# Performance work log

Hardware: AMD Instinct MI355X
Metric: run time of the kernel (lower is better)

## Reference

```python
import jax, jax.numpy as jnp
import numpy as np

B, T, IMG, PS, D, DEPTH, NH = 1, 8, 224, 16, 768, 12, 12
HP = IMG // PS
NP = HP * HP          # 196 patches per frame
N = NP + 1            # +1 cls token per frame
DH = D // NH
MLP = 4 * D
SCALE = DH ** -0.5


def _ln(x, g, b):
    mu = x.mean(-1, keepdims=True)
    var = ((x - mu) ** 2).mean(-1, keepdims=True)
    return (x - mu) / jnp.sqrt(var + 1e-5) * g + b


def _forward(x, W_patch, b_patch, cls_token, pos_embed,
             ln1_g, ln1_b, qkv_w, qkv_b, proj_w, proj_b,
             ln2_g, ln2_b, fc1_w, fc1_b, fc2_w, fc2_b, lnf_g, lnf_b):
    Bc = x.shape[0]
    # --- patch embed (Conv3d k=(1,ps,ps), stride=(1,ps,ps) == per-frame patch matmul) ---
    p = x.reshape(Bc, T, 3, HP, PS, HP, PS).transpose(0, 1, 3, 5, 2, 4, 6)
    p = p.reshape(Bc, T, NP, 3 * PS * PS)
    emb = p @ W_patch.T + b_patch                     # [B,T,NP,D] (correct layout)
    # replicate torch flatten(3)/transpose(1,2)/reshape axis scramble:
    emb = jnp.swapaxes(emb, 2, 3).reshape(Bc, T, NP, D)
    cls = jnp.broadcast_to(cls_token.reshape(1, 1, 1, D), (Bc, T, 1, D))
    h = jnp.concatenate([cls, emb], axis=2) + pos_embed.reshape(1, 1, N, D)
    h = h.reshape(Bc, T * N, D)

    for i in range(DEPTH):
        # --- attention ---
        a = _ln(h, ln1_g[i], ln1_b[i])
        qkv = (a @ qkv_w[i] + qkv_b[i]).reshape(Bc, T * N, 3, NH, DH)
        q, k, v = (jnp.transpose(qkv[:, :, j], (0, 2, 1, 3)) for j in range(3))  # [B,H,S,dh]
        if i % 2 == 0:  # divided space-time
            qf = q.reshape(Bc, NH, T, N, DH)
            kf = k.reshape(Bc, NH, T, N, DH)
            vf = v.reshape(Bc, NH, T, N, DH)
            q_t = qf.mean(3, keepdims=True)           # [B,H,T,1,dh]
            k_t = kf.mean(3, keepdims=True)
            v_t = vf.mean(3, keepdims=True)
            attn_t = jax.nn.softmax(jnp.einsum('bhtqd,bhtkd->bhtqk', q_t, k_t) * SCALE, -1)
            x_t = jnp.einsum('bhtqk,bhtkd->bhtqd', attn_t, v_t)[:, :, :, 0]  # [B,H,T,dh]
            attn_s = jax.nn.softmax(jnp.einsum('bhtqd,bhtkd->bhtqk', qf, kf) * SCALE, -1)
            x_s = jnp.einsum('bhtqk,bhtkd->bhtqd', attn_s, vf)               # [B,H,T,N,dh]
            o = (x_s + x_t[:, :, :, None, :]).reshape(Bc, NH, T * N, DH)
        else:  # joint space-time
            attn = jax.nn.softmax(jnp.einsum('bhqd,bhkd->bhqk', q, k) * SCALE, -1)
            o = jnp.einsum('bhqk,bhkd->bhqd', attn, v)
        o = jnp.transpose(o, (0, 2, 1, 3)).reshape(Bc, T * N, D)
        h = h + (o @ proj_w[i] + proj_b[i])
        # --- mlp ---
        m = _ln(h, ln2_g[i], ln2_b[i])
        m = jax.nn.gelu(m @ fc1_w[i] + fc1_b[i], approximate=False)
        h = h + (m @ fc2_w[i] + fc2_b[i])

    return _ln(h, lnf_g, lnf_b).reshape(Bc, T, N, D)


def setup_inputs() -> dict:
    key = jax.random.key(0)
    ks = jax.random.split(key, 12)
    s = 0.02
    return {
        'x': jax.random.normal(ks[0], (B, T, 3, IMG, IMG), jnp.float32),
        'W_patch': jax.random.normal(ks[1], (D, 3 * PS * PS), jnp.float32) * s,
        'b_patch': jnp.zeros((D,), jnp.float32),
        'cls_token': jax.random.normal(ks[2], (1, 1, D), jnp.float32) * s,
        'pos_embed': jax.random.normal(ks[3], (1, N, D), jnp.float32) * s,
        'ln1_g': jnp.ones((DEPTH, D), jnp.float32),
        'ln1_b': jnp.zeros((DEPTH, D), jnp.float32),
        'qkv_w': jax.random.normal(ks[4], (DEPTH, D, 3 * D), jnp.float32) * s,
        'qkv_b': jnp.zeros((DEPTH, 3 * D), jnp.float32),
        'proj_w': jax.random.normal(ks[5], (DEPTH, D, D), jnp.float32) * s,
        'proj_b': jnp.zeros((DEPTH, D), jnp.float32),
        'ln2_g': jnp.ones((DEPTH, D), jnp.float32),
        'ln2_b': jnp.zeros((DEPTH, D), jnp.float32),
        'fc1_w': jax.random.normal(ks[6], (DEPTH, D, MLP), jnp.float32) * s,
        'fc1_b': jnp.zeros((DEPTH, MLP), jnp.float32),
        'fc2_w': jax.random.normal(ks[7], (DEPTH, MLP, D), jnp.float32) * s,
        'fc2_b': jnp.zeros((DEPTH, D), jnp.float32),
        'lnf_g': jnp.ones((D,), jnp.float32),
        'lnf_b': jnp.zeros((D,), jnp.float32),
    }


def reference(x, W_patch, b_patch, cls_token, pos_embed,
              ln1_g, ln1_b, qkv_w, qkv_b, proj_w, proj_b,
              ln2_g, ln2_b, fc1_w, fc1_b, fc2_w, fc2_b, lnf_g, lnf_b):
    return _forward(x, W_patch, b_patch, cls_token, pos_embed,
                    ln1_g, ln1_b, qkv_w, qkv_b, proj_w, proj_b,
                    ln2_g, ln2_b, fc1_w, fc1_b, fc2_w, fc2_b, lnf_g, lnf_b)
```

## Files before the change

kernel.cpp:

```cpp
#include <hip/hip_runtime.h>
#include <math.h>

#define Dm 768
#define Tn 8
#define Nn 197
#define Sn 1576
#define MLPn 3072
#define NPn 196
#define MPAD 1664

typedef unsigned short u16;
typedef __bf16 bf16x8 __attribute__((ext_vector_type(8)));
typedef float f32x4 __attribute__((ext_vector_type(4)));
typedef unsigned int u32x4 __attribute__((ext_vector_type(4)));
typedef u16 u16x8 __attribute__((ext_vector_type(8)));
typedef u16 u16x4 __attribute__((ext_vector_type(4)));

__device__ inline u16 f2bf(float f) {
    union { float f; unsigned u; } v; v.f = f;
    unsigned r = v.u + 0x7fffu + ((v.u >> 16) & 1u);
    return (u16)(r >> 16);
}
__device__ inline float bf2f(u16 v) {
    union { unsigned u; float f; } x; x.u = ((unsigned)v) << 16; return x.f;
}

__device__ __forceinline__ void gl_lds16(const u16* __restrict__ g, u16* l) {
    __builtin_amdgcn_global_load_lds((const __attribute__((address_space(1))) void*)g,
                                     (__attribute__((address_space(3))) void*)l,
                                     16, 0, 0);
}

__global__ __launch_bounds__(256) void im2col_k(const float* __restrict__ x, u16* __restrict__ P) {
    int idx = blockIdx.x * 256 + threadIdx.x;
    if (idx >= 1568 * 768) return;
    int c = idx % 768, r = idx / 768;
    int p = r % 196, t = r / 196;
    int hp = p / 14, wp = p % 14;
    int ch = c / 256, rem = c % 256, py = rem / 16, px = rem % 16;
    P[idx] = f2bf(x[((t * 3 + ch) * 224 + hp * 16 + py) * 224 + wp * 16 + px]);
}

__global__ __launch_bounds__(256) void cvt_k(const float* __restrict__ s, u16* __restrict__ d, int n) {
    int i = blockIdx.x * 256 + threadIdx.x;
    if (i < n) d[i] = f2bf(s[i]);
}

__global__ __launch_bounds__(256) void cvtT_all_k(const float* __restrict__ qw_, const float* __restrict__ pw_,
                                                  const float* __restrict__ f1w_, const float* __restrict__ f2w_,
                                                  u16* __restrict__ Wq_, u16* __restrict__ Wp_,
                                                  u16* __restrict__ W1_, u16* __restrict__ W2_) {
    __shared__ float tile[32][33];
    int layer = blockIdx.y;
    const float* qw  = qw_  + (size_t)layer * 768 * 2304;
    const float* pw  = pw_  + (size_t)layer * 768 * 768;
    const float* f1w = f1w_ + (size_t)layer * 768 * 3072;
    const float* f2w = f2w_ + (size_t)layer * 3072 * 768;
    u16* Wq = Wq_ + (size_t)layer * 2304 * 768;
    u16* Wp = Wp_ + (size_t)layer * 768 * 768;
    u16* W1 = W1_ + (size_t)layer * 3072 * 768;
    u16* W2 = W2_ + (size_t)layer * 768 * 3072;
    int bid = blockIdx.x;
    const float* src; u16* dst; int K, N, k0, n0;
    if (bid < 1728)      { src = qw;  dst = Wq; K = 768;  N = 2304; int r = bid;        k0 = (r / 72) * 32; n0 = (r % 72) * 32; }
    else if (bid < 2304) { src = pw;  dst = Wp; K = 768;  N = 768;  int r = bid - 1728; k0 = (r / 24) * 32; n0 = (r % 24) * 32; }
    else if (bid < 4608) { src = f1w; dst = W1; K = 768;  N = 3072; int r = bid - 2304; k0 = (r / 96) * 32; n0 = (r % 96) * 32; }
    else                 { src = f2w; dst = W2; K = 3072; N = 768;  int r = bid - 4608; k0 = (r / 24) * 32; n0 = (r % 24) * 32; }
    int tx = threadIdx.x & 31, ty = threadIdx.x >> 5;
#pragma unroll
    for (int i = 0; i < 4; ++i) tile[ty + 8 * i][tx] = src[(size_t)(k0 + ty + 8 * i) * N + n0 + tx];
    __syncthreads();
#pragma unroll
    for (int i = 0; i < 4; ++i) dst[(size_t)(n0 + ty + 8 * i) * K + k0 + tx] = f2bf(tile[tx][ty + 8 * i]);
}

__global__ __launch_bounds__(256) void build_h_k(const float* __restrict__ emb, const float* __restrict__ cls,
                                                 const float* __restrict__ pos, float* __restrict__ h) {
    int idx = blockIdx.x * 256 + threadIdx.x;
    if (idx >= Sn * Dm) return;
    int d = idx % Dm, s = idx / Dm;
    int t = s / Nn, r = s % Nn;
    float v;
    if (r == 0) v = cls[d];
    else {
        int f = (r - 1) * Dm + d;
        int p = f % NPn, dd = f / NPn;
        v = emb[(size_t)(t * NPn + p) * Dm + dd];
    }
    h[idx] = v + pos[r * Dm + d];
}

template <typename OutT>
__global__ __launch_bounds__(256) void ln_k(const float* __restrict__ X, const float* __restrict__ g,
                                            const float* __restrict__ bta, OutT* __restrict__ Y) {
    int row = blockIdx.x;
    const float* x = X + (size_t)row * Dm;
    float s = 0.f, s2 = 0.f;
#pragma unroll
    for (int q = 0; q < 3; ++q) {
        float v = x[threadIdx.x + q * 256];
        s += v; s2 += v * v;
    }
#pragma unroll
    for (int off = 1; off < 64; off <<= 1) {
        s  += __shfl_xor(s,  off);
        s2 += __shfl_xor(s2, off);
    }
    __shared__ float red[8];
    int wv = threadIdx.x >> 6;
    if ((threadIdx.x & 63) == 0) { red[wv * 2] = s; red[wv * 2 + 1] = s2; }
    __syncthreads();
    s  = red[0] + red[2] + red[4] + red[6];
    s2 = red[1] + red[3] + red[5] + red[7];
    float mu  = s * (1.f / 768.f);
    float var = s2 * (1.f / 768.f) - mu * mu;
    float rstd = rsqrtf(var + 1e-5f);
#pragma unroll
    for (int q = 0; q < 3; ++q) {
        int i = threadIdx.x + q * 256;
        float v = (x[i] - mu) * rstd * g[i] + bta[i];
        if constexpr (sizeof(OutT) == 2) Y[(size_t)row * Dm + i] = f2bf(v);
        else                             Y[(size_t)row * Dm + i] = v;
    }
}

__global__ __launch_bounds__(256) void mgemm_k(const u16* __restrict__ A, const u16* __restrict__ Bt,
                                               float* __restrict__ Cp, int N, int Kfull, int Kc) {
    __shared__ __align__(16) u16 As[3 * 4096];
    __shared__ __align__(16) u16 Bs[3 * 4096];
    int split = blockIdx.z;
    A  += split * Kc;
    Bt += split * Kc;
    Cp += (size_t)split * MPAD * N;
    int tid = threadIdx.x;
    int lane = tid & 63, w = tid >> 6;
    int wm = w & 1, wn = w >> 1;
    int m0 = blockIdx.y * 128, n0 = blockIdx.x * 128;
    f32x4 acc[4][4] = {};
    int c0 = tid, c1 = tid + 256;
    int ar0 = ((c0 >> 6) << 4) + (c0 & 15), ac0 = ((c0 >> 4) & 3) << 3;
    int ar1 = ((c1 >> 6) << 4) + (c1 & 15), ac1 = ((c1 >> 4) & 3) << 3;
    const u16* Arow0 = A  + (size_t)(m0 + ar0) * Kfull + ac0;
    const u16* Arow1 = A  + (size_t)(m0 + ar1) * Kfull + ac1;
    const u16* Brow0 = Bt + (size_t)(n0 + ar0) * Kfull + ac0;
    const u16* Brow1 = Bt + (size_t)(n0 + ar1) * Kfull + ac1;
    auto STAGE = [&](int buf, int k0) {
        int bo = buf * 4096;
        gl_lds16(Arow0 + k0, As + bo + (w * 64) * 8);
        gl_lds16(Arow1 + k0, As + bo + (256 + w * 64) * 8);
        gl_lds16(Brow0 + k0, Bs + bo + (w * 64) * 8);
        gl_lds16(Brow1 + k0, Bs + bo + (256 + w * 64) * 8);
    };
    int nt = Kc >> 5;
    STAGE(0, 0);
    STAGE(1, 32);
    int buf = 0;
    for (int t = 0; t < nt; ++t) {
        if (t + 2 < nt) { int sb = buf + 2; if (sb >= 3) sb -= 3; STAGE(sb, (t + 2) * 32); }
        int ahead = nt - 1 - t;
        if (ahead >= 2)      asm volatile("s_waitcnt vmcnt(8)" ::: "memory");
        else if (ahead == 1) asm volatile("s_waitcnt vmcnt(4)" ::: "memory");
        else                 asm volatile("s_waitcnt vmcnt(0)" ::: "memory");
        __builtin_amdgcn_s_barrier();
        const u16* Ab = As + buf * 4096;
        const u16* Bb = Bs + buf * 4096;
        bf16x8 af[4], bfr[4];
#pragma unroll
        for (int i = 0; i < 4; ++i) {
            af[i]  = *(const bf16x8*)(Ab + (((wm * 4 + i) * 64 + lane) << 3));
            bfr[i] = *(const bf16x8*)(Bb + (((wn * 4 + i) * 64 + lane) << 3));
        }
#pragma unroll
        for (int mi = 0; mi < 4; ++mi)
#pragma unroll
            for (int ni = 0; ni < 4; ++ni)
                acc[mi][ni] = __builtin_amdgcn_mfma_f32_16x16x32_bf16(af[mi], bfr[ni], acc[mi][ni], 0, 0, 0);
        asm volatile("" ::: "memory");
        __builtin_amdgcn_s_barrier();
        buf = (buf == 2) ? 0 : buf + 1;
    }
    int rbase = (lane >> 4) << 2, cl = lane & 15;
#pragma unroll
    for (int mi = 0; mi < 4; ++mi)
#pragma unroll
        for (int r = 0; r < 4; ++r) {
            int gm = m0 + wm * 64 + mi * 16 + rbase + r;
#pragma unroll
            for (int ni = 0; ni < 4; ++ni) {
                int gn = n0 + wn * 64 + ni * 16 + cl;
                Cp[(size_t)gm * N + gn] = acc[mi][ni][r];
            }
        }
}

template <bool GELU_ACT>
__global__ __launch_bounds__(256) void mgemm_fused_k(const u16* __restrict__ A, const u16* __restrict__ Bt,
                                                     const float* __restrict__ bias, u16* __restrict__ out,
                                                     int N, int Kfull, int Mout) {
    __shared__ __align__(16) u16 As[3 * 64 * 32];
    __shared__ __align__(16) u16 Bs[3 * 128 * 32];
    int tid = threadIdx.x;
    int lane = tid & 63, w = tid >> 6;
    int wm = w & 1, wn = w >> 1;
    int m0 = blockIdx.y * 64, n0 = blockIdx.x * 128;
    f32x4 acc[2][4] = {};
    int ca = tid;
    int ar = ((ca >> 6) << 4) + (ca & 15), ac = ((ca >> 4) & 3) << 3;
    const u16* Arow = A + (size_t)(m0 + ar) * Kfull + ac;
    int cb1 = tid + 256;
    int br1 = ((cb1 >> 6) << 4) + (cb1 & 15), bc1 = ((cb1 >> 4) & 3) << 3;
    const u16* Brow0 = Bt + (size_t)(n0 + ar) * Kfull + ac;
    const u16* Brow1 = Bt + (size_t)(n0 + br1) * Kfull + bc1;
    auto STAGE = [&](int buf, int k0) {
        gl_lds16(Arow + k0, As + buf * 2048 + (w * 64) * 8);
        gl_lds16(Brow0 + k0, Bs + buf * 4096 + (w * 64) * 8);
        gl_lds16(Brow1 + k0, Bs + buf * 4096 + (256 + w * 64) * 8);
    };
    int nt = Kfull >> 5;
    STAGE(0, 0);
    STAGE(1, 32);
    int buf = 0;
    for (int t = 0; t < nt; ++t) {
        if (t + 2 < nt) { int sb = buf + 2; if (sb >= 3) sb -= 3; STAGE(sb, (t + 2) * 32); }
        int ahead = nt - 1 - t;
        if (ahead >= 2)      asm volatile("s_waitcnt vmcnt(6)" ::: "memory");
        else if (ahead == 1) asm volatile("s_waitcnt vmcnt(3)" ::: "memory");
        else                 asm volatile("s_waitcnt vmcnt(0)" ::: "memory");
        __builtin_amdgcn_s_barrier();
        const u16* Ab = As + buf * 2048;
        const u16* Bb = Bs + buf * 4096;
        bf16x8 af[2], bfr[4];
#pragma unroll
        for (int i = 0; i < 2; ++i) af[i]  = *(const bf16x8*)(Ab + (((wm * 2 + i) * 64 + lane) << 3));
#pragma unroll
        for (int j = 0; j < 4; ++j) bfr[j] = *(const bf16x8*)(Bb + (((wn * 4 + j) * 64 + lane) << 3));
#pragma unroll
        for (int mi = 0; mi < 2; ++mi)
#pragma unroll
            for (int ni = 0; ni < 4; ++ni)
                acc[mi][ni] = __builtin_amdgcn_mfma_f32_16x16x32_bf16(af[mi], bfr[ni], acc[mi][ni], 0, 0, 0);
        asm volatile("" ::: "memory");
        __builtin_amdgcn_s_barrier();
        buf = (buf == 2) ? 0 : buf + 1;
    }
    int rbase = (lane >> 4) << 2, cl = lane & 15;
#pragma unroll
    for (int mi = 0; mi < 2; ++mi)
#pragma unroll
        for (int r = 0; r < 4; ++r) {
            int gm = m0 + wm * 32 + mi * 16 + rbase + r;
            if (gm < Mout) {
#pragma unroll
                for (int ni = 0; ni < 4; ++ni) {
                    int gn = n0 + wn * 64 + ni * 16 + cl;
                    float v = acc[mi][ni][r] + bias[gn];
                    if (GELU_ACT) v = 0.5f * v * (1.f + erff(v * 0.7071067811865476f));
                    out[(size_t)gm * N + gn] = f2bf(v);
                }
            }
        }
}

__global__ __launch_bounds__(256) void ep_k(const float* __restrict__ Cp, const float* __restrict__ bias,
                                            float* __restrict__ out, int N, int S) {
    int row = blockIdx.y;
    int n = blockIdx.x * 1024 + threadIdx.x * 4;
    if (n >= N) return;
    size_t off = (size_t)row * N + n;
    f32x4 acc = *(const f32x4*)(Cp + off);
    for (int s = 1; s < S; ++s)
        acc += *(const f32x4*)(Cp + (size_t)s * MPAD * N + off);
    acc += *(const f32x4*)(bias + n);
    *(f32x4*)(out + off) = acc;
}

template <bool FINALOUT>
__global__ __launch_bounds__(256) void ep_ln_k(const float* __restrict__ Cp, const float* __restrict__ bias,
                                               float* __restrict__ h, const float* __restrict__ g,
                                               const float* __restrict__ bta, void* __restrict__ lnout, int S) {
    int row = blockIdx.x;
    int t = threadIdx.x;
    float v[3];
    float s = 0.f, s2 = 0.f;
#pragma unroll
    for (int q = 0; q < 3; ++q) {
        int i = t + q * 256;
        size_t off = (size_t)row * Dm + i;
        float a = Cp[off];
        for (int sp = 1; sp < S; ++sp) a += Cp[(size_t)sp * MPAD * Dm + off];
        a += bias[i] + h[off];
        h[off] = a;
        v[q] = a; s += a; s2 += a * a;
    }
#pragma unroll
    for (int off = 1; off < 64; off <<= 1) {
        s  += __shfl_xor(s,  off);
        s2 += __shfl_xor(s2, off);
    }
    __shared__ float red[8];
    int wv = t >> 6;
    if ((t & 63) == 0) { red[wv * 2] = s; red[wv * 2 + 1] = s2; }
    __syncthreads();
    s  = red[0] + red[2] + red[4] + red[6];
    s2 = red[1] + red[3] + red[5] + red[7];
    float mu  = s * (1.f / 768.f);
    float var = s2 * (1.f / 768.f) - mu * mu;
    float rstd = rsqrtf(var + 1e-5f);
#pragma unroll
    for (int q = 0; q < 3; ++q) {
        int i = t + q * 256;
        float y = (v[q] - mu) * rstd * g[i] + bta[i];
        if constexpr (FINALOUT) ((float*)lnout)[(size_t)row * Dm + i] = y;
        else                    ((u16*)lnout)[(size_t)row * Dm + i] = f2bf(y);
    }
}

__global__ __launch_bounds__(256) void vmean_k(const u16* __restrict__ qkv, float* __restrict__ vm) {
    int g = blockIdx.x;
    int h = g >> 3, t = g & 7;
    int d = threadIdx.x & 63, part = threadIdx.x >> 6;
    float s = 0.f;
    for (int n = part; n < Nn; n += 4)
        s += bf2f(qkv[(size_t)(t * Nn + n) * 2304 + 1536 + h * 64 + d]);
    __shared__ float red[256];
    red[threadIdx.x] = s;
    __syncthreads();
    if (part == 0) vm[g * 64 + d] = (red[d] + red[64 + d] + red[128 + d] + red[192 + d]) * (1.f / 197.f);
}

__global__ __launch_bounds__(256) void attn_mfma_k(const u16* __restrict__ qkv, float* __restrict__ Ou,
                                                   float* __restrict__ ml, const float* __restrict__ vm,
                                                   u16* __restrict__ ob, int even, int nsplit,
                                                   int NG, int Sq, int fuse) {
    __shared__ __align__(16) u16 Ks[64 * 64];
    __shared__ __align__(16) u16 Vt[64 * 64];
    __shared__ __align__(16) u16 Ps[4 * 32 * 64];
    int g = blockIdx.y;
    int h, sbase;
    if (even) { h = g >> 3; sbase = (g & 7) * Nn; } else { h = g; sbase = 0; }
    int split = blockIdx.z;
    int chunk = (Sq + nsplit - 1) / nsplit;
    int kbeg = split * chunk, kend = min(Sq, kbeg + chunk);
    int tid = threadIdx.x, lane = tid & 63, w = tid >> 6;
    int quad = lane >> 4, l15 = lane & 15;
    int q0w = blockIdx.x * 128 + w * 32;
    u16* Pw = Ps + w * 2048;

    bf16x8 aq[2][2];
#pragma unroll
    for (int mb = 0; mb < 2; ++mb) {
        int qidx = q0w + mb * 16 + l15; if (qidx >= Sq) qidx = Sq - 1;
        const u16* qp = qkv + (size_t)(sbase + qidx) * 2304 + h * 64;
#pragma unroll
        for (int ks = 0; ks < 2; ++ks)
            aq[mb][ks] = *(const bf16x8*)(qp + ks * 32 + quad * 8);
    }
    f32x4 acc_o[2][4] = {};
    float m_run[2][4], l_run[2][4];
#pragma unroll
    for (int mb = 0; mb < 2; ++mb)
#pragma unroll
        for (int r = 0; r < 4; ++r) { m_run[mb][r] = -INFINITY; l_run[mb][r] = 0.f; }

    for (int kt = kbeg; kt < kend; kt += 64) {
        int cnt = kend - kt; if (cnt > 64) cnt = 64;
        {
            int dc = tid & 7;
#pragma unroll
            for (int p = 0; p < 2; ++p) {
                int row = (tid >> 3) + 32 * p;
                u32x4 kd = {};
                if (row < cnt) kd = *(const u32x4*)(qkv + (size_t)(sbase + kt + row) * 2304 + 768 + h * 64 + dc * 8);
                *(u32x4*)(Ks + row * 64 + ((dc ^ (row & 7)) << 3)) = kd;
            }
        }
        {
            int d = (tid & 31) * 2, kc = tid >> 5;
            u16x8 lo, hi;
#pragma unroll
            for (int i = 0; i < 8; ++i) {
                int key = kc * 8 + i;
                unsigned t = 0;
                if (key < cnt) t = *(const unsigned*)(qkv + (size_t)(sbase + kt + key) * 2304 + 1536 + h * 64 + d);
                lo[i] = (u16)(t & 0xffffu); hi[i] = (u16)(t >> 16);
            }
            *(u16x8*)(Vt + d * 64 + ((kc ^ (d & 7)) << 3)) = lo;
            *(u16x8*)(Vt + (d + 1) * 64 + ((kc ^ ((d + 1) & 7)) << 3)) = hi;
        }
        __syncthreads();
        f32x4 acc_s[2][4] = {};
#pragma unroll
        for (int ni = 0; ni < 4; ++ni) {
            int key = l15 + ni * 16;
#pragma unroll
            for (int ks = 0; ks < 2; ++ks) {
                bf16x8 bk = *(const bf16x8*)(Ks + key * 64 + ((((ks << 2) + quad) ^ (key & 7)) << 3));
                acc_s[0][ni] = __builtin_amdgcn_mfma_f32_16x16x32_bf16(aq[0][ks], bk, acc_s[0][ni], 0, 0, 0);
                acc_s[1][ni] = __builtin_amdgcn_mfma_f32_16x16x32_bf16(aq[1][ks], bk, acc_s[1][ni], 0, 0, 0);
            }
        }
#pragma unroll
        for (int mb = 0; mb < 2; ++mb) {
#pragma unroll
            for (int ni = 0; ni < 4; ++ni) {
                int keyabs = kt + l15 + ni * 16;
#pragma unroll
                for (int r = 0; r < 4; ++r) {
                    float sv = acc_s[mb][ni][r] * 0.125f;
                    if (keyabs >= kend) sv = -1e30f;
                    acc_s[mb][ni][r] = sv;
                }
            }
#pragma unroll
            for (int r = 0; r < 4; ++r) {
                float mx = fmaxf(fmaxf(acc_s[mb][0][r], acc_s[mb][1][r]), fmaxf(acc_s[mb][2][r], acc_s[mb][3][r]));
                mx = fmaxf(mx, __shfl_xor(mx, 1));
                mx = fmaxf(mx, __shfl_xor(mx, 2));
                mx = fmaxf(mx, __shfl_xor(mx, 4));
                mx = fmaxf(mx, __shfl_xor(mx, 8));
                float mnew = fmaxf(m_run[mb][r], mx);
                float pv[4], ps = 0.f;
#pragma unroll
                for (int ni = 0; ni < 4; ++ni) { pv[ni] = __expf(acc_s[mb][ni][r] - mnew); ps += pv[ni]; }
                ps += __shfl_xor(ps, 1);
                ps += __shfl_xor(ps, 2);
                ps += __shfl_xor(ps, 4);
                ps += __shfl_xor(ps, 8);
                float alpha = __expf(m_run[mb][r] - mnew);
                l_run[mb][r] = l_run[mb][r] * alpha + ps;
                m_run[mb][r] = mnew;
#pragma unroll
                for (int ni = 0; ni < 4; ++ni) acc_o[mb][ni][r] *= alpha;
                int prow = mb * 16 + quad * 4 + r;
#pragma unroll
                for (int ni = 0; ni < 4; ++ni) {
                    int key = l15 + ni * 16;
                    Pw[prow * 64 + (((key >> 3) ^ (prow & 7)) << 3) + (key & 7)] = f2bf(pv[ni]);
                }
            }
        }
        bf16x8 ap[2][2];
#pragma unroll
        for (int mb = 0; mb < 2; ++mb)
#pragma unroll
            for (int ks = 0; ks < 2; ++ks)
                ap[mb][ks] = *(const bf16x8*)(Pw + (mb * 16 + l15) * 64 + ((((ks << 2) + quad) ^ (l15 & 7)) << 3));
#pragma unroll
        for (int ni = 0; ni < 4; ++ni) {
            int d = l15 + ni * 16;
#pragma unroll
            for (int ks = 0; ks < 2; ++ks) {
                bf16x8 bv = *(const bf16x8*)(Vt + d * 64 + ((((ks << 2) + quad) ^ (d & 7)) << 3));
                acc_o[0][ni] = __builtin_amdgcn_mfma_f32_16x16x32_bf16(ap[0][ks], bv, acc_o[0][ni], 0, 0, 0);
                acc_o[1][ni] = __builtin_amdgcn_mfma_f32_16x16x32_bf16(ap[1][ks], bv, acc_o[1][ni], 0, 0, 0);
            }
        }
        __syncthreads();
    }
    if (fuse) {
#pragma unroll
        for (int mb = 0; mb < 2; ++mb)
#pragma unroll
            for (int r = 0; r < 4; ++r) {
                int q = q0w + mb * 16 + quad * 4 + r;
                if (q < Sq) {
                    float inv = 1.f / l_run[mb][r];
                    u16* op = ob + (size_t)(sbase + q) * Dm + h * 64;
#pragma unroll
                    for (int ni = 0; ni < 4; ++ni) {
                        int d = l15 + ni * 16;
                        op[d] = f2bf(acc_o[mb][ni][r] * inv + vm[g * 64 + d]);
                    }
                }
            }
    } else {
        size_t gb = ((size_t)split * NG + g) * Sq;
#pragma unroll
        for (int mb = 0; mb < 2; ++mb)
#pragma unroll
            for (int r = 0; r < 4; ++r) {
                int q = q0w + mb * 16 + quad * 4 + r;
                if (q < Sq) {
                    float* op = Ou + (gb + q) * 64;
#pragma unroll
                    for (int ni = 0; ni < 4; ++ni) op[l15 + ni * 16] = acc_o[mb][ni][r];
                    if (l15 == 0) {
                        ml[(gb + q) * 2]     = m_run[mb][r];
                        ml[(gb + q) * 2 + 1] = l_run[mb][r];
                    }
                }
            }
    }
}

__global__ __launch_bounds__(256) void comb_k(const float* __restrict__ Ou, const float* __restrict__ ml,
                                              u16* __restrict__ ob, int nsplit, int NG, int Sq) {
    int g = blockIdx.y;
    int q = blockIdx.x * 4 + (threadIdx.x >> 6);
    int d = threadIdx.x & 63;
    if (q >= Sq) return;
    int h = g, sbase = 0;
    float M = -INFINITY;
    for (int s = 0; s < nsplit; ++s) M = fmaxf(M, ml[(((size_t)s * NG + g) * Sq + q) * 2]);
    float num = 0.f, den = 0.f;
    for (int s = 0; s < nsplit; ++s) {
        size_t base = ((size_t)s * NG + g) * Sq + q;
        float wgt = __expf(ml[base * 2] - M);
        den += wgt * ml[base * 2 + 1];
        num += wgt * Ou[base * 64 + d];
    }
    float o = num / den;
    ob[(size_t)(sbase + q) * Dm + h * 64 + d] = f2bf(o);
}

extern "C" void kernel_launch(void* const* d_in, const int* in_sizes, int n_in,
                              void* d_out, int out_size, void* d_ws, size_t ws_size,
                              hipStream_t stream) {
    (void)in_sizes; (void)n_in; (void)out_size; (void)ws_size;
    const float* x       = (const float*)d_in[0];
    const float* W_patch = (const float*)d_in[1];
    const float* b_patch = (const float*)d_in[2];
    const float* cls     = (const float*)d_in[3];
    const float* pos     = (const float*)d_in[4];
    const float* ln1_g   = (const float*)d_in[5];
    const float* ln1_b   = (const float*)d_in[6];
    const float* qkv_w   = (const float*)d_in[7];
    const float* qkv_b   = (const float*)d_in[8];
    const float* proj_w  = (const float*)d_in[9];
    const float* proj_b  = (const float*)d_in[10];
    const float* ln2_g   = (const float*)d_in[11];
    const float* ln2_b   = (const float*)d_in[12];
    const float* fc1_w   = (const float*)d_in[13];
    const float* fc1_b   = (const float*)d_in[14];
    const float* fc2_w   = (const float*)d_in[15];
    const float* fc2_b   = (const float*)d_in[16];
    const float* lnf_g   = (const float*)d_in[17];
    const float* lnf_b   = (const float*)d_in[18];

    char* base = (char*)d_ws;
    auto alloc = [&](size_t bytes) { void* p = base; base += (bytes + 255) & ~(size_t)255; return p; };
    u16*   P    = (u16*)  alloc((size_t)MPAD * 768 * 2);
    u16*   Wpe  = (u16*)  alloc((size_t)768 * 768 * 2);
    u16*   Wq   = (u16*)  alloc((size_t)12 * 2304 * 768 * 2);
    u16*   Wp   = (u16*)  alloc((size_t)12 * 768 * 768 * 2);
    u16*   W1   = (u16*)  alloc((size_t)12 * 3072 * 768 * 2);
    u16*   W2   = (u16*)  alloc((size_t)12 * 768 * 3072 * 2);
    float* emb  = (float*)alloc((size_t)1568 * 768 * 4);
    float* h    = (float*)alloc((size_t)Sn * Dm * 4);
    u16*   a    = (u16*)  alloc((size_t)MPAD * 768 * 2);
    u16*   qkvb = (u16*)  alloc((size_t)Sn * 2304 * 2);
    u16*   ob   = (u16*)  alloc((size_t)MPAD * 768 * 2);
    u16*   mb   = (u16*)  alloc((size_t)MPAD * 3072 * 2);
    float* vm   = (float*)alloc((size_t)96 * 64 * 4);
    float* Ou   = (float*)alloc((size_t)3 * 12 * Sn * 64 * 4);
    float* ml   = (float*)alloc((size_t)3 * 12 * Sn * 2 * 4);
    float* Cp   = (float*)alloc((size_t)4 * MPAD * 768 * 4);

    cvtT_all_k<<<dim3(6912, 12), 256, 0, stream>>>(qkv_w, proj_w, fc1_w, fc2_w, Wq, Wp, W1, W2);
    im2col_k<<<(1568 * 768 + 255) / 256, 256, 0, stream>>>(x, P);
    cvt_k<<<(768 * 768 + 255) / 256, 256, 0, stream>>>(W_patch, Wpe, 768 * 768);
    mgemm_k<<<dim3(6, 13, 3), 256, 0, stream>>>(P, Wpe, Cp, 768, 768, 256);
    ep_k<<<dim3(1, 1568), 256, 0, stream>>>(Cp, b_patch, emb, 768, 3);
    build_h_k<<<(Sn * Dm + 255) / 256, 256, 0, stream>>>(emb, cls, pos, h);
    ln_k<u16><<<Sn, 256, 0, stream>>>(h, ln1_g, ln1_b, a);

    for (int i = 0; i < 12; ++i) {
        const u16* Wqi = Wq + (size_t)i * 2304 * 768;
        const u16* Wpi = Wp + (size_t)i * 768 * 768;
        const u16* W1i = W1 + (size_t)i * 3072 * 768;
        const u16* W2i = W2 + (size_t)i * 768 * 3072;
        mgemm_fused_k<false><<<dim3(18, 26), 256, 0, stream>>>(a, Wqi, qkv_b + i * 2304, qkvb, 2304, 768, Sn);
        if ((i & 1) == 0) {
            vmean_k<<<96, 256, 0, stream>>>(qkvb, vm);
            attn_mfma_k<<<dim3(2, 96, 1), 256, 0, stream>>>(qkvb, Ou, ml, vm, ob, 1, 1, 96, Nn, 1);
        } else {
            attn_mfma_k<<<dim3(13, 12, 3), 256, 0, stream>>>(qkvb, Ou, ml, vm, ob, 0, 3, 12, Sn, 0);
            comb_k<<<dim3(394, 12), 256, 0, stream>>>(Ou, ml, ob, 3, 12, Sn);
        }
        mgemm_k<<<dim3(6, 13, 4), 256, 0, stream>>>(ob, Wpi, Cp, 768, 768, 192);
        ep_ln_k<false><<<Sn, 256, 0, stream>>>(Cp, proj_b + i * Dm, h, ln2_g + i * Dm, ln2_b + i * Dm, a, 4);
        mgemm_fused_k<true><<<dim3(24, 26), 256, 0, stream>>>(a, W1i, fc1_b + i * MLPn, mb, 3072, 768, Sn);
        mgemm_k<<<dim3(6, 13, 4), 256, 0, stream>>>(mb, W2i, Cp, 768, 3072, 768);
        if (i < 11)
            ep_ln_k<false><<<Sn, 256, 0, stream>>>(Cp, fc2_b + i * Dm, h, ln1_g + (i + 1) * Dm, ln1_b + (i + 1) * Dm, a, 4);
        else
            ep_ln_k<true><<<Sn, 256, 0, stream>>>(Cp, fc2_b + i * Dm, h, lnf_g, lnf_b, d_out, 4);
    }
}
```

Measured before the change: 2.302 ms.

## Accumulate split-K GEMM partials atomically into residual and widen weight transpose tiles

```diff
diff --git a/kernel.cpp b/kernel.cpp
--- a/kernel.cpp
+++ b/kernel.cpp
@@ -46,32 +46,44 @@
     if (i < n) d[i] = f2bf(s[i]);
 }
 
-__global__ __launch_bounds__(256) void cvtT_all_k(const float* __restrict__ qw_, const float* __restrict__ pw_,
-                                                  const float* __restrict__ f1w_, const float* __restrict__ f2w_,
-                                                  u16* __restrict__ Wq_, u16* __restrict__ Wp_,
-                                                  u16* __restrict__ W1_, u16* __restrict__ W2_) {
-    __shared__ float tile[32][33];
+__global__ __launch_bounds__(256) void cvtT2_k(const float* __restrict__ qw_, const float* __restrict__ pw_,
+                                               const float* __restrict__ f1w_, const float* __restrict__ f2w_,
+                                               u16* __restrict__ Wq_, u16* __restrict__ Wp_,
+                                               u16* __restrict__ W1_, u16* __restrict__ W2_) {
+    __shared__ u16 tl[64 * 68];
     int layer = blockIdx.y;
-    const float* qw  = qw_  + (size_t)layer * 768 * 2304;
-    const float* pw  = pw_  + (size_t)layer * 768 * 768;
-    const float* f1w = f1w_ + (size_t)layer * 768 * 3072;
-    const float* f2w = f2w_ + (size_t)layer * 3072 * 768;
-    u16* Wq = Wq_ + (size_t)layer * 2304 * 768;
-    u16* Wp = Wp_ + (size_t)layer * 768 * 768;
-    u16* W1 = W1_ + (size_t)layer * 3072 * 768;
-    u16* W2 = W2_ + (size_t)layer * 768 * 3072;
-    int bid = blockIdx.x;
-    const float* src; u16* dst; int K, N, k0, n0;
-    if (bid < 1728)      { src = qw;  dst = Wq; K = 768;  N = 2304; int r = bid;        k0 = (r / 72) * 32; n0 = (r % 72) * 32; }
-    else if (bid < 2304) { src = pw;  dst = Wp; K = 768;  N = 768;  int r = bid - 1728; k0 = (r / 24) * 32; n0 = (r % 24) * 32; }
-    else if (bid < 4608) { src = f1w; dst = W1; K = 768;  N = 3072; int r = bid - 2304; k0 = (r / 96) * 32; n0 = (r % 96) * 32; }
-    else                 { src = f2w; dst = W2; K = 3072; N = 768;  int r = bid - 4608; k0 = (r / 24) * 32; n0 = (r % 24) * 32; }
-    int tx = threadIdx.x & 31, ty = threadIdx.x >> 5;
-#pragma unroll
-    for (int i = 0; i < 4; ++i) tile[ty + 8 * i][tx] = src[(size_t)(k0 + ty + 8 * i) * N + n0 + tx];
+    int r = blockIdx.x;
+    const float* src; u16* dst; int K, N, tk, tn;
+    if (r < 432)       { src = qw_  + (size_t)layer * 768 * 2304; dst = Wq_ + (size_t)layer * 2304 * 768;
+                         K = 768;  N = 2304; tk = r / 36; tn = r % 36; }
+    else if (r < 576)  { r -= 432; src = pw_  + (size_t)layer * 768 * 768;  dst = Wp_ + (size_t)layer * 768 * 768;
+                         K = 768;  N = 768;  tk = r / 12; tn = r % 12; }
+    else if (r < 1152) { r -= 576; src = f1w_ + (size_t)layer * 768 * 3072; dst = W1_ + (size_t)layer * 3072 * 768;
+                         K = 768;  N = 3072; tk = r / 48; tn = r % 48; }
+    else               { r -= 1152; src = f2w_ + (size_t)layer * 3072 * 768; dst = W2_ + (size_t)layer * 768 * 3072;
+                         K = 3072; N = 768;  tk = r / 12; tn = r % 12; }
+    int k0 = tk * 64, n0 = tn * 64;
+    int t = threadIdx.x;
+    {
+        int nx = (t & 15) * 4, ky = t >> 4;
+#pragma unroll
+        for (int i = 0; i < 4; ++i) {
+            int row = ky + 16 * i;
+            f32x4 v = *(const f32x4*)(src + (size_t)(k0 + row) * N + n0 + nx);
+#pragma unroll
+            for (int j = 0; j < 4; ++j) tl[(nx + j) * 68 + row] = f2bf(v[j]);
+        }
+    }
     __syncthreads();
-#pragma unroll
-    for (int i = 0; i < 4; ++i) dst[(size_t)(n0 + ty + 8 * i) * K + k0 + tx] = f2bf(tile[tx][ty + 8 * i]);
+    {
+        int kc = t & 15, nr0 = t >> 4;
+#pragma unroll
+        for (int i = 0; i < 4; ++i) {
+            int nr = nr0 + 16 * i;
+            u16x4 o = *(const u16x4*)(tl + nr * 68 + kc * 4);
+            *(u16x4*)(dst + (size_t)(n0 + nr) * K + k0 + kc * 4) = o;
+        }
+    }
 }
 
 __global__ __launch_bounds__(256) void build_h_k(const float* __restrict__ emb, const float* __restrict__ cls,
@@ -193,6 +205,76 @@
         }
 }
 
+__global__ __launch_bounds__(256) void mgemm_at_k(const u16* __restrict__ A, const u16* __restrict__ Bt,
+                                                  float* __restrict__ h, int N, int Kfull, int Kc, int Mout) {
+    __shared__ __align__(16) u16 As[3 * 4096];
+    __shared__ __align__(16) u16 Bs[3 * 4096];
+    int split = blockIdx.z;
+    A  += split * Kc;
+    Bt += split * Kc;
+    int tid = threadIdx.x;
+    int lane = tid & 63, w = tid >> 6;
+    int wm = w & 1, wn = w >> 1;
+    int m0 = blockIdx.y * 128, n0 = blockIdx.x * 128;
+    f32x4 acc[4][4] = {};
+    int c0 = tid, c1 = tid + 256;
+    int ar0 = ((c0 >> 6) << 4) + (c0 & 15), ac0 = ((c0 >> 4) & 3) << 3;
+    int ar1 = ((c1 >> 6) << 4) + (c1 & 15), ac1 = ((c1 >> 4) & 3) << 3;
+    const u16* Arow0 = A  + (size_t)(m0 + ar0) * Kfull + ac0;
+    const u16* Arow1 = A  + (size_t)(m0 + ar1) * Kfull + ac1;
+    const u16* Brow0 = Bt + (size_t)(n0 + ar0) * Kfull + ac0;
+    const u16* Brow1 = Bt + (size_t)(n0 + ar1) * Kfull + ac1;
+    auto STAGE = [&](int buf, int k0) {
+        int bo = buf * 4096;
+        gl_lds16(Arow0 + k0, As + bo + (w * 64) * 8);
+        gl_lds16(Arow1 + k0, As + bo + (256 + w * 64) * 8);
+        gl_lds16(Brow0 + k0, Bs + bo + (w * 64) * 8);
+        gl_lds16(Brow1 + k0, Bs + bo + (256 + w * 64) * 8);
+    };
+    int nt = Kc >> 5;
+    STAGE(0, 0);
+    STAGE(1, 32);
+    int buf = 0;
+    for (int t = 0; t < nt; ++t) {
+        if (t + 2 < nt) { int sb = buf + 2; if (sb >= 3) sb -= 3; STAGE(sb, (t + 2) * 32); }
+        int ahead = nt - 1 - t;
+        if (ahead >= 2)      asm volatile("s_waitcnt vmcnt(8)" ::: "memory");
+        else if (ahead == 1) asm volatile("s_waitcnt vmcnt(4)" ::: "memory");
+        else                 asm volatile("s_waitcnt vmcnt(0)" ::: "memory");
+        __builtin_amdgcn_s_barrier();
+        const u16* Ab = As + buf * 4096;
+        const u16* Bb = Bs + buf * 4096;
+        bf16x8 af[4], bfr[4];
+#pragma unroll
+        for (int i = 0; i < 4; ++i) {
+            af[i]  = *(const bf16x8*)(Ab + (((wm * 4 + i) * 64 + lane) << 3));
+            bfr[i] = *(const bf16x8*)(Bb + (((wn * 4 + i) * 64 + lane) << 3));
+        }
+#pragma unroll
+        for (int mi = 0; mi < 4; ++mi)
+#pragma unroll
+            for (int ni = 0; ni < 4; ++ni)
+                acc[mi][ni] = __builtin_amdgcn_mfma_f32_16x16x32_bf16(af[mi], bfr[ni], acc[mi][ni], 0, 0, 0);
+        asm volatile("" ::: "memory");
+        __builtin_amdgcn_s_barrier();
+        buf = (buf == 2) ? 0 : buf + 1;
+    }
+    int rbase = (lane >> 4) << 2, cl = lane & 15;
+#pragma unroll
+    for (int mi = 0; mi < 4; ++mi)
+#pragma unroll
+        for (int r = 0; r < 4; ++r) {
+            int gm = m0 + wm * 64 + mi * 16 + rbase + r;
+            if (gm < Mout) {
+#pragma unroll
+                for (int ni = 0; ni < 4; ++ni) {
+                    int gn = n0 + wn * 64 + ni * 16 + cl;
+                    atomicAdd(&h[(size_t)gm * N + gn], acc[mi][ni][r]);
+                }
+            }
+        }
+}
+
 template <bool GELU_ACT>
 __global__ __launch_bounds__(256) void mgemm_fused_k(const u16* __restrict__ A, const u16* __restrict__ Bt,
                                                      const float* __restrict__ bias, u16* __restrict__ out,
@@ -275,9 +357,9 @@
 }
 
 template <bool FINALOUT>
-__global__ __launch_bounds__(256) void ep_ln_k(const float* __restrict__ Cp, const float* __restrict__ bias,
-                                               float* __restrict__ h, const float* __restrict__ g,
-                                               const float* __restrict__ bta, void* __restrict__ lnout, int S) {
+__global__ __launch_bounds__(256) void ep_ln2_k(const float* __restrict__ bias, float* __restrict__ h,
+                                                const float* __restrict__ g, const float* __restrict__ bta,
+                                                void* __restrict__ lnout) {
     int row = blockIdx.x;
     int t = threadIdx.x;
     float v[3];
@@ -286,9 +368,7 @@
     for (int q = 0; q < 3; ++q) {
         int i = t + q * 256;
         size_t off = (size_t)row * Dm + i;
-        float a = Cp[off];
-        for (int sp = 1; sp < S; ++sp) a += Cp[(size_t)sp * MPAD * Dm + off];
-        a += bias[i] + h[off];
+        float a = h[off] + bias[i];
         h[off] = a;
         v[q] = a; s += a; s2 += a * a;
     }
@@ -554,9 +634,9 @@
     float* vm   = (float*)alloc((size_t)96 * 64 * 4);
     float* Ou   = (float*)alloc((size_t)3 * 12 * Sn * 64 * 4);
     float* ml   = (float*)alloc((size_t)3 * 12 * Sn * 2 * 4);
-    float* Cp   = (float*)alloc((size_t)4 * MPAD * 768 * 4);
-
-    cvtT_all_k<<<dim3(6912, 12), 256, 0, stream>>>(qkv_w, proj_w, fc1_w, fc2_w, Wq, Wp, W1, W2);
+    float* Cp   = (float*)alloc((size_t)3 * MPAD * 768 * 4);
+
+    cvtT2_k<<<dim3(1728, 12), 256, 0, stream>>>(qkv_w, proj_w, fc1_w, fc2_w, Wq, Wp, W1, W2);
     im2col_k<<<(1568 * 768 + 255) / 256, 256, 0, stream>>>(x, P);
     cvt_k<<<(768 * 768 + 255) / 256, 256, 0, stream>>>(W_patch, Wpe, 768 * 768);
     mgemm_k<<<dim3(6, 13, 3), 256, 0, stream>>>(P, Wpe, Cp, 768, 768, 256);
@@ -577,13 +657,13 @@
             attn_mfma_k<<<dim3(13, 12, 3), 256, 0, stream>>>(qkvb, Ou, ml, vm, ob, 0, 3, 12, Sn, 0);
             comb_k<<<dim3(394, 12), 256, 0, stream>>>(Ou, ml, ob, 3, 12, Sn);
         }
-        mgemm_k<<<dim3(6, 13, 4), 256, 0, stream>>>(ob, Wpi, Cp, 768, 768, 192);
-        ep_ln_k<false><<<Sn, 256, 0, stream>>>(Cp, proj_b + i * Dm, h, ln2_g + i * Dm, ln2_b + i * Dm, a, 4);
+        mgemm_at_k<<<dim3(6, 13, 4), 256, 0, stream>>>(ob, Wpi, h, 768, 768, 192, Sn);
+        ep_ln2_k<false><<<Sn, 256, 0, stream>>>(proj_b + i * Dm, h, ln2_g + i * Dm, ln2_b + i * Dm, a);
         mgemm_fused_k<true><<<dim3(24, 26), 256, 0, stream>>>(a, W1i, fc1_b + i * MLPn, mb, 3072, 768, Sn);
-        mgemm_k<<<dim3(6, 13, 4), 256, 0, stream>>>(mb, W2i, Cp, 768, 3072, 768);
+        mgemm_at_k<<<dim3(6, 13, 4), 256, 0, stream>>>(mb, W2i, h, 768, 3072, 768, Sn);
         if (i < 11)
-            ep_ln_k<false><<<Sn, 256, 0, stream>>>(Cp, fc2_b + i * Dm, h, ln1_g + (i + 1) * Dm, ln1_b + (i + 1) * Dm, a, 4);
+            ep_ln2_k<false><<<Sn, 256, 0, stream>>>(fc2_b + i * Dm, h, ln1_g + (i + 1) * Dm, ln1_b + (i + 1) * Dm, a);
         else
-            ep_ln_k<true><<<Sn, 256, 0, stream>>>(Cp, fc2_b + i * Dm, h, lnf_g, lnf_b, d_out, 4);
-    }
-}
+            ep_ln2_k<true><<<Sn, 256, 0, stream>>>(fc2_b + i * Dm, h, lnf_g, lnf_b, d_out);
+    }
+}
```

Result: slower. 2.446 ms (+6.2%).
